# Performance work log

Measured on AMD Instinct MI355X. Metric: run time of the kernel, lower is better.

Reference implementation:

```python
import jax, jax.numpy as jnp
import numpy as np

DILATION = 6
KS = 3
N = KS * KS  # 9 kernel sample points
PAD = 1      # zero padding inside DeformConv2d
EPS = 1e-5


def conv2d(x, w, b=None, padding=0):
    out = jax.lax.conv_general_dilated(
        x, w, window_strides=(1, 1),
        padding=[(padding, padding), (padding, padding)],
        dimension_numbers=('NCHW', 'OIHW', 'NCHW'))
    if b is not None:
        out = out + b[None, :, None, None]
    return out


def batchnorm_train(x, gamma, beta):
    # training-mode BN (module default): batch statistics over (N,H,W)
    mean = x.mean(axis=(0, 2, 3), keepdims=True)
    var = x.var(axis=(0, 2, 3), keepdims=True)
    return gamma[None, :, None, None] * (x - mean) * jax.lax.rsqrt(var + EPS) + beta[None, :, None, None]


def deform_conv(x, p_w, p_b, m_w, m_b, d_w, d_b, w):
    b, c, h, wd = x.shape
    offset = conv2d(x, p_w, p_b, padding=1)                 # (b, 2N, h, w)
    m = jax.nn.sigmoid(conv2d(x, m_w, m_b, padding=1))      # (b, N, h, w) modulation
    s = 2.0 * jax.nn.sigmoid(conv2d(x, d_w, d_b, padding=1))  # (b,1,h,w) adaptive dilation scale (=1 at logit 0)
    xp = jnp.pad(x, ((0, 0), (0, 0), (PAD, PAD), (PAD, PAD)))
    Hp, Wp = h + 2 * PAD, wd + 2 * PAD
    # kernel grid p_n, row-major (kh, kw) to match conv weight layout
    rng = jnp.arange(-(KS - 1) // 2, (KS - 1) // 2 + 1, dtype=x.dtype)
    pn_x, pn_y = jnp.meshgrid(rng, rng, indexing='ij')
    pn_x, pn_y = pn_x.reshape(-1), pn_y.reshape(-1)          # (N,)
    # base sampling positions (offset by PAD into padded map)
    p0_x = jnp.arange(1, h + 1, dtype=x.dtype)[:, None, None]    # (h,1,1)
    p0_y = jnp.arange(1, wd + 1, dtype=x.dtype)[None, :, None]   # (1,w,1)
    off = offset.transpose(0, 2, 3, 1)   # (b,h,w,2N)
    s_ = s.transpose(0, 2, 3, 1)         # (b,h,w,1)
    px = p0_x + DILATION * s_ * pn_x + off[..., :N]   # (b,h,w,N)
    py = p0_y + DILATION * s_ * pn_y + off[..., N:]
    fx, fy = jnp.floor(px), jnp.floor(py)
    qx_lt = jnp.clip(fx, 0, Hp - 1).astype(jnp.int32)
    qy_lt = jnp.clip(fy, 0, Wp - 1).astype(jnp.int32)
    qx_rb = jnp.clip(fx + 1, 0, Hp - 1).astype(jnp.int32)
    qy_rb = jnp.clip(fy + 1, 0, Wp - 1).astype(jnp.int32)
    pxc = jnp.clip(px, 0, Hp - 1)
    pyc = jnp.clip(py, 0, Wp - 1)
    g_lt = (1 + (qx_lt - pxc)) * (1 + (qy_lt - pyc))
    g_rb = (1 - (qx_rb - pxc)) * (1 - (qy_rb - pyc))
    g_lb = (1 + (qx_lt - pxc)) * (1 - (qy_rb - pyc))
    g_rt = (1 - (qx_rb - pxc)) * (1 + (qy_lt - pyc))

    def gather(qx, qy):
        idx = (qx * Wp + qy).reshape(b, 1, -1)                    # (b,1,h*w*N)
        xf = xp.reshape(b, c, Hp * Wp)
        out = jnp.take_along_axis(xf, jnp.broadcast_to(idx, (b, c, idx.shape[-1])), axis=2)
        return out.reshape(b, c, h, wd, N)

    x_off = (g_lt[:, None] * gather(qx_lt, qy_lt)
             + g_rb[:, None] * gather(qx_rb, qy_rb)
             + g_lb[:, None] * gather(qx_lt, qy_rb)
             + g_rt[:, None] * gather(qx_rb, qy_lt))
    x_off = x_off * m.transpose(0, 2, 3, 1)[:, None]              # modulation
    # final 3x3 conv over gathered samples == contraction over (c, N)
    return jnp.einsum('bchwn,ocn->bohw', x_off, w.reshape(w.shape[0], c, N))


def setup_inputs() -> dict:
    key = jax.random.key(0)
    ks = jax.random.split(key, 12)
    cin, c1, c2 = 512, 256, 64
    b, h, w = 2, 96, 96
    def rn(k, shape, scale):
        return jax.random.normal(k, shape, dtype=jnp.float32) * scale
    return {
        'x': rn(ks[0], (b, cin, h, w), 1.0),
        'bn1_g': jnp.ones((cin,), jnp.float32),
        'bn1_b': jnp.zeros((cin,), jnp.float32),
        'conv1_w': rn(ks[1], (c1, cin, 1, 1), (1.0 / cin) ** 0.5),
        'conv1_b': jnp.zeros((c1,), jnp.float32),
        'bn2_g': jnp.ones((c1,), jnp.float32),
        'bn2_b': jnp.zeros((c1,), jnp.float32),
        'p_w': rn(ks[2], (2 * N, c1, 3, 3), 0.01),
        'p_b': jnp.zeros((2 * N,), jnp.float32),
        'm_w': rn(ks[3], (N, c1, 3, 3), 0.01),
        'm_b': jnp.zeros((N,), jnp.float32),
        'd_w': rn(ks[4], (1, c1, 3, 3), 0.01),
        'd_b': jnp.zeros((1,), jnp.float32),
        'dconv_w': rn(ks[5], (c2, c1, 3, 3), (1.0 / (c1 * 9)) ** 0.5),
    }


def reference(x, bn1_g, bn1_b, conv1_w, conv1_b, bn2_g, bn2_b,
              p_w, p_b, m_w, m_b, d_w, d_b, dconv_w):
    f = jax.nn.relu(batchnorm_train(x, bn1_g, bn1_b))
    f = conv2d(f, conv1_w, conv1_b)
    f = batchnorm_train(f, bn2_g, bn2_b)
    return deform_conv(f, p_w, p_b, m_w, m_b, d_w, d_b, dconv_w)
```

## Files before the change

### kernel.cpp

```cpp
#include <hip/hip_runtime.h>
#include <hip/hip_bf16.h>
#include <math.h>

#define BATCH 2
#define CIN 512
#define C1 256
#define C2 64
#define HH 96
#define WW 96
#define HWSZ 9216
#define NPIX 18432
#define HP 98
#define WP 98
#define PLSTRIDE 516096

typedef __attribute__((ext_vector_type(8))) short bf16x8;
typedef __attribute__((ext_vector_type(4))) short bf16x4;
typedef __attribute__((ext_vector_type(4))) float f32x4;
typedef __attribute__((ext_vector_type(4))) unsigned int u32x4;
typedef __attribute__((ext_vector_type(2))) unsigned int u32x2;
typedef unsigned short u16;
typedef unsigned int u32;

__device__ __forceinline__ float bfu2f(u16 u) {
  u32 v = ((u32)u) << 16; return __builtin_bit_cast(float, v);
}
__device__ __forceinline__ u16 f2bfu(float f) {
  return __builtin_bit_cast(u16, __float2bfloat16(f));
}
__device__ __forceinline__ float rd_any(const void* p, size_t i, int fl) {
  return fl ? bfu2f(((const u16*)p)[i]) : ((const float*)p)[i];
}
__device__ __forceinline__ int get_fl(const u32* g1raw) {
  return g1raw[0] != 0x3F800000u;
}
__device__ __forceinline__ bf16x8 lds_frag(const u16* p) {
  bf16x4 lo = *(const bf16x4*)p;
  bf16x4 hi = *(const bf16x4*)(p + 4);
  bf16x8 r;
  r[0] = lo[0]; r[1] = lo[1]; r[2] = lo[2]; r[3] = lo[3];
  r[4] = hi[0]; r[5] = hi[1]; r[6] = hi[2]; r[7] = hi[3];
  return r;
}
__device__ __forceinline__ void split4(const f32x4& v, u32x2& ph, u32x2& pl) {
  u16 h0 = f2bfu(v[0]), h1 = f2bfu(v[1]), h2 = f2bfu(v[2]), h3 = f2bfu(v[3]);
  u16 l0 = f2bfu(v[0] - bfu2f(h0)), l1 = f2bfu(v[1] - bfu2f(h1));
  u16 l2 = f2bfu(v[2] - bfu2f(h2)), l3 = f2bfu(v[3] - bfu2f(h3));
  ph = (u32x2){(u32)h0 | ((u32)h1 << 16), (u32)h2 | ((u32)h3 << 16)};
  pl = (u32x2){(u32)l0 | ((u32)l1 << 16), (u32)l2 | ((u32)l3 << 16)};
}

__global__ __launch_bounds__(256) void prep_kernel(
    const void* cw, const void* pw, const void* mw, const void* dw, const void* dcw,
    const void* cb, const void* g1, const void* b1, const void* g2, const void* b2,
    const void* pb, const void* mb, const void* db,
    u16* __restrict__ W1b, u16* __restrict__ W1l,
    u16* __restrict__ Wofa, u16* __restrict__ Wofal,
    u16* __restrict__ Wab, u16* __restrict__ Wabl,
    float* __restrict__ canon, float* __restrict__ statz) {
  int e = blockIdx.x * 256 + threadIdx.x;
  if (e >= 356380) return;
  int fl = get_fl((const u32*)g1);
  if (e < 131072) {
    float v = rd_any(cw, e, fl);
    u16 h = f2bfu(v);
    W1b[e] = h; W1l[e] = f2bfu(v - bfu2f(h));
  } else if (e < 204800) {
    int i = e - 131072;
    int tap = i >> 13; int r = i & 8191; int m = r >> 8; int c = r & 255;
    float v = 0.f;
    if (m < 18)       v = rd_any(pw, (size_t)(m * 256 + c) * 9 + tap, fl);
    else if (m < 27)  v = rd_any(mw, (size_t)((m - 18) * 256 + c) * 9 + tap, fl);
    else if (m == 27) v = rd_any(dw, (size_t)c * 9 + tap, fl);
    u16 h = f2bfu(v);
    Wofa[i] = h; Wofal[i] = f2bfu(v - bfu2f(h));
  } else if (e < 352256) {
    int i = e - 204800;
    int n = i >> 14; int r = i & 16383; int o = r >> 8; int c = r & 255;
    float v = rd_any(dcw, (size_t)(o * 256 + c) * 9 + n, fl);
    u16 h = f2bfu(v);
    Wab[i] = h; Wabl[i] = f2bfu(v - bfu2f(h));
  } else if (e < 354076) {
    int i = e - 352256;
    const void* src; int off;
    if      (i < 256)  { src = cb; off = i; }
    else if (i < 768)  { src = g1; off = i - 256; }
    else if (i < 1280) { src = b1; off = i - 768; }
    else if (i < 1536) { src = g2; off = i - 1280; }
    else if (i < 1792) { src = b2; off = i - 1536; }
    else if (i < 1810) { src = pb; off = i - 1792; }
    else if (i < 1819) { src = mb; off = i - 1810; }
    else               { src = db; off = i - 1819; }
    canon[i] = rd_any(src, off, fl);
  } else {
    statz[e - 354076] = 0.f;
  }
}

__global__ __launch_bounds__(256) void bn_stats_kernel(
    const void* __restrict__ x, const float* __restrict__ gamma,
    const float* __restrict__ beta, float* __restrict__ scale,
    float* __restrict__ shift, float* __restrict__ sums, float* __restrict__ sumsq,
    int* __restrict__ cnt, const u32* __restrict__ g1raw, int force, int C) {
  int c = blockIdx.x, part = blockIdx.y, tid = threadIdx.x;
  int fl = force ? 1 : get_fl(g1raw);
  int b = part >> 1, half = part & 1;
  size_t base = ((size_t)(b * C + c)) * HWSZ + half * (HWSZ / 2);
  float s = 0.f, q = 0.f;
  if (fl) {
    const u16* p = (const u16*)x + base;
    for (int i = tid; i < 576; i += 256) {
      u32x4 U = *(const u32x4*)(p + i * 8);
      #pragma unroll
      for (int k = 0; k < 4; ++k) {
        float v0 = bfu2f((u16)(U[k] & 0xffff));
        float v1 = bfu2f((u16)(U[k] >> 16));
        s += v0 + v1; q = fmaf(v0, v0, fmaf(v1, v1, q));
      }
    }
  } else {
    const float* p = (const float*)x + base;
    for (int i = tid; i < 1152; i += 256) {
      f32x4 v = *(const f32x4*)(p + i * 4);
      #pragma unroll
      for (int k = 0; k < 4; ++k) { s += v[k]; q = fmaf(v[k], v[k], q); }
    }
  }
  __shared__ float sh[512];
  sh[tid] = s; sh[tid + 256] = q;
  __syncthreads();
  for (int off = 128; off > 0; off >>= 1) {
    if (tid < off) { sh[tid] += sh[tid + off]; sh[tid + 256] += sh[tid + 256 + off]; }
    __syncthreads();
  }
  if (tid == 0) {
    atomicAdd(&sums[c], sh[0]);
    atomicAdd(&sumsq[c], sh[256]);
    __threadfence();
    int old = atomicAdd(&cnt[c], 1);
    if (old == 3) {
      float S = atomicAdd(&sums[c], 0.f);
      float Q = atomicAdd(&sumsq[c], 0.f);
      float mean = S * (1.f / (float)NPIX);
      float var  = fmaxf(Q * (1.f / (float)NPIX) - mean * mean, 0.f);
      float sc = gamma[c] * rsqrtf(var + 1e-5f);
      scale[c] = sc;
      shift[c] = beta[c] - mean * sc;
    }
  }
}

__global__ __launch_bounds__(256) void conv1x1_kernel(
    const void* __restrict__ x, const u16* __restrict__ W1b, const u16* __restrict__ W1l,
    const float* __restrict__ cb, const float* __restrict__ scale,
    const float* __restrict__ shift, const u32* __restrict__ g1raw,
    u16* __restrict__ f1) {
  __shared__ u16 Bh[2][64][68];
  __shared__ u16 Bl[2][64][68];
  int tid = threadIdx.x;
  int fl = get_fl(g1raw);
  int bxr = blockIdx.x;
  int bx = (bxr & 7) * 36 + (bxr >> 3);
  int p0 = bx * 64;
  int co0 = blockIdx.y * 128;
  int b = p0 / HWSZ;
  int hw0 = p0 % HWSZ;
  int lane = tid & 63, wv = tid >> 6, quad = lane >> 4, mr = lane & 15;
  int m0 = co0 + wv * 32;
  f32x4 acc[2][4];
  #pragma unroll
  for (int i = 0; i < 2; ++i)
    #pragma unroll
    for (int j = 0; j < 4; ++j) acc[i][j] = (f32x4){0.f, 0.f, 0.f, 0.f};

  int spx = tid & 63, cg = tid >> 6;
  int gpx = hw0 + spx;

  float pva[8], pvb[8];
  auto ISSUE = [&](int c0) {
    #pragma unroll
    for (int j = 0; j < 8; ++j) {
      int ci = c0 + cg * 16 + j * 2;
      if (fl) {
        const u16* xb = (const u16*)x;
        pva[j] = bfu2f(xb[((size_t)(b * CIN + ci)) * HWSZ + gpx]);
        pvb[j] = bfu2f(xb[((size_t)(b * CIN + ci + 1)) * HWSZ + gpx]);
      } else {
        const float* xf = (const float*)x;
        pva[j] = xf[((size_t)(b * CIN + ci)) * HWSZ + gpx];
        pvb[j] = xf[((size_t)(b * CIN + ci + 1)) * HWSZ + gpx];
      }
    }
  };
  auto COMBINE = [&](int buf, int c0) {
    #pragma unroll
    for (int j = 0; j < 8; ++j) {
      int ci = c0 + cg * 16 + j * 2;
      float v0 = fmaxf(fmaf(pva[j], scale[ci], shift[ci]), 0.f);
      float v1 = fmaxf(fmaf(pvb[j], scale[ci + 1], shift[ci + 1]), 0.f);
      u16 h0 = f2bfu(v0), h1 = f2bfu(v1);
      u16 l0 = f2bfu(v0 - bfu2f(h0)), l1 = f2bfu(v1 - bfu2f(h1));
      *(u32*)&Bh[buf][spx][cg * 16 + j * 2] = (u32)h0 | ((u32)h1 << 16);
      *(u32*)&Bl[buf][spx][cg * 16 + j * 2] = (u32)l0 | ((u32)l1 << 16);
    }
  };

  ISSUE(0);
  COMBINE(0, 0);
  for (int c8 = 0; c8 < 8; ++c8) {
    __syncthreads();
    if (c8 < 7) ISSUE((c8 + 1) * 64);
    int bsel = c8 & 1;
    int c0 = c8 * 64;
    #pragma unroll
    for (int kk2 = 0; kk2 < 2; ++kk2) {
      int kk = kk2 * 32;
      #pragma unroll
      for (int mf = 0; mf < 2; ++mf) {
        size_t wix = (size_t)(m0 + mf * 16 + mr) * CIN + c0 + kk + quad * 8;
        bf16x8 ah = *(const bf16x8*)(W1b + wix);
        bf16x8 al = *(const bf16x8*)(W1l + wix);
        #pragma unroll
        for (int nt = 0; nt < 4; ++nt) {
          bf16x8 bl = lds_frag(&Bl[bsel][nt * 16 + mr][kk + quad * 8]);
          bf16x8 bh = lds_frag(&Bh[bsel][nt * 16 + mr][kk + quad * 8]);
          acc[mf][nt] = __builtin_amdgcn_mfma_f32_16x16x32_bf16(ah, bl, acc[mf][nt], 0, 0, 0);
          acc[mf][nt] = __builtin_amdgcn_mfma_f32_16x16x32_bf16(al, bh, acc[mf][nt], 0, 0, 0);
          acc[mf][nt] = __builtin_amdgcn_mfma_f32_16x16x32_bf16(ah, bh, acc[mf][nt], 0, 0, 0);
        }
      }
    }
    if (c8 < 7) COMBINE(bsel ^ 1, (c8 + 1) * 64);
  }
  #pragma unroll
  for (int mf = 0; mf < 2; ++mf) {
    #pragma unroll
    for (int nt = 0; nt < 4; ++nt) {
      #pragma unroll
      for (int r = 0; r < 4; ++r) {
        int co = m0 + mf * 16 + quad * 4 + r;
        f1[((size_t)(b * C1 + co)) * HWSZ + hw0 + nt * 16 + mr] = f2bfu(acc[mf][nt][r] + cb[co]);
      }
    }
  }
}

__global__ __launch_bounds__(256) void bn2pad_kernel(
    const u16* __restrict__ f1, const float* __restrict__ scale,
    const float* __restrict__ shift, float* __restrict__ xpf) {
  int bid = blockIdx.x;
  int ht = bid % 144; int ct = (bid / 144) & 3; int b = bid / 576;
  int hw0 = ht * 64, c0 = ct * 64;
  __shared__ float t[64][65];
  int tid = threadIdx.x;
  #pragma unroll
  for (int it = 0; it < 16; ++it) {
    int e = it * 256 + tid;
    int p = e & 63, ci = e >> 6;
    float v = bfu2f(f1[((size_t)(b * C1 + c0 + ci)) * HWSZ + hw0 + p]);
    t[ci][p] = fmaf(v, scale[c0 + ci], shift[c0 + ci]);
  }
  __syncthreads();
  #pragma unroll
  for (int it = 0; it < 16; ++it) {
    int e = it * 256 + tid;
    int ci = e & 63, p = e >> 6;
    int hw = hw0 + p; int h = hw / WW; int w = hw % WW;
    xpf[(((size_t)(b * HP) + h + 1) * WP + w + 1) * C1 + c0 + ci] = t[ci][p];
  }
}

__global__ __launch_bounds__(256) void init_kernel(float* __restrict__ xpf) {
  int k = blockIdx.x * 256 + threadIdx.x;
  int ch = k & 255; int pxi = k >> 8;
  int bb = pxi / 388; int r = pxi % 388;
  int h, w;
  if (r < 98)      { h = 0;  w = r; }
  else if (r < 196){ h = 97; w = r - 98; }
  else if (r < 292){ h = r - 196 + 1; w = 0; }
  else             { h = r - 292 + 1; w = 97; }
  xpf[(((size_t)(bb * HP) + h) * WP + w) * C1 + ch] = 0.f;
}

__global__ __launch_bounds__(256) void offconv_kernel(
    const float* __restrict__ xpf, const u16* __restrict__ Wofa, const u16* __restrict__ Wofal,
    const float* __restrict__ pbc, const float* __restrict__ mbc,
    const float* __restrict__ dbc, float* __restrict__ opart3) {
  __shared__ u16 Vh[2][32][68];
  __shared__ u16 Vl[2][32][68];
  int tid = threadIdx.x;
  int bxr = blockIdx.x;
  int bx = (bxr & 7) * 72 + (bxr >> 3);
  int tg = blockIdx.y;
  int p0 = bx * 32;
  int b = p0 / HWSZ;
  int hw = p0 % HWSZ; int h0 = hw / WW; int w0 = hw % WW;
  int lane = tid & 63, wv = tid >> 6, quad = lane >> 4, mr = lane & 15;
  int m0 = (wv & 1) * 16;
  int ntile = wv >> 1;
  int srow = tid >> 4;
  int scol = (tid & 15) * 4;
  f32x4 acc = (f32x4){0.f, 0.f, 0.f, 0.f};

  f32x4 pv[2];
  auto ISSUE = [&](int it) {
    int tap = tg * 3 + (it >> 2);
    int th = tap / 3, tw = tap % 3;
    int c0 = (it & 3) * 64;
    const float* base = xpf + ((size_t)(b * HP + h0 + th) * WP + (w0 + tw)) * C1;
    #pragma unroll
    for (int pass = 0; pass < 2; ++pass) {
      int px = pass * 16 + srow;
      pv[pass] = *(const f32x4*)(base + (size_t)px * C1 + c0 + scol);
    }
  };
  auto COMBINE = [&](int buf) {
    #pragma unroll
    for (int pass = 0; pass < 2; ++pass) {
      int px = pass * 16 + srow;
      u32x2 ph, pl;
      split4(pv[pass], ph, pl);
      *(u32x2*)&Vh[buf][px][scol] = ph;
      *(u32x2*)&Vl[buf][px][scol] = pl;
    }
  };

  ISSUE(0);
  COMBINE(0);
  for (int it = 0; it < 12; ++it) {
    __syncthreads();
    if (it < 11) ISSUE(it + 1);
    int bsel = it & 1;
    int tap = tg * 3 + (it >> 2);
    int c0 = (it & 3) * 64;
    #pragma unroll
    for (int kk2 = 0; kk2 < 2; ++kk2) {
      int kof = kk2 * 32 + quad * 8;
      size_t wix = (size_t)(tap * 32 + m0 + mr) * C1 + c0 + kof;
      bf16x8 ah = *(const bf16x8*)(Wofa + wix);
      bf16x8 al = *(const bf16x8*)(Wofal + wix);
      bf16x8 bl = lds_frag(&Vl[bsel][ntile * 16 + mr][kof]);
      bf16x8 bh = lds_frag(&Vh[bsel][ntile * 16 + mr][kof]);
      acc = __builtin_amdgcn_mfma_f32_16x16x32_bf16(ah, bl, acc, 0, 0, 0);
      acc = __builtin_amdgcn_mfma_f32_16x16x32_bf16(al, bh, acc, 0, 0, 0);
      acc = __builtin_amdgcn_mfma_f32_16x16x32_bf16(ah, bh, acc, 0, 0, 0);
    }
    if (it < 11) COMBINE(bsel ^ 1);
  }
  float* plane = opart3 + (size_t)tg * PLSTRIDE;
  int px = ntile * 16 + mr;
  #pragma unroll
  for (int r = 0; r < 4; ++r) {
    int m = m0 + quad * 4 + r;
    if (m < 28) {
      float v = acc[r];
      if (tg == 0) v += (m < 18) ? pbc[m] : ((m < 27) ? mbc[m - 18] : dbc[0]);
      plane[(size_t)m * NPIX + p0 + px] = v;
    }
  }
}

__global__ __launch_bounds__(256) void deform_kernel(
    const float* __restrict__ xpf, const u16* __restrict__ Wab, const u16* __restrict__ Wabl,
    const float* __restrict__ opart3, float* __restrict__ planes3) {
  __shared__ u16   Vh[2][32][68];
  __shared__ u16   Vl[2][32][68];
  __shared__ int   smi[3][4][32];
  __shared__ float smw[3][4][32];
  int tid = threadIdx.x;
  int bxr = blockIdx.x;
  int bx = (bxr & 7) * 72 + (bxr >> 3);
  int g = blockIdx.y;
  int p0 = bx * 32;
  int b = p0 / HWSZ;
  int hw0 = p0 % HWSZ;

  if (tid < 96) {
    int nn = tid >> 5;
    int p = tid & 31;
    int n = g * 3 + nn;
    int bp = p0 + p;
    int hw = hw0 + p; int h = hw / WW; int w = hw % WW;
    const float* P0 = opart3;
    const float* P1 = opart3 + PLSTRIDE;
    const float* P2 = opart3 + 2 * PLSTRIDE;
    size_t iox = (size_t)n * NPIX + bp;
    size_t ioy = (size_t)(9 + n) * NPIX + bp;
    size_t iml = (size_t)(18 + n) * NPIX + bp;
    size_t isl = (size_t)27 * NPIX + bp;
    float offx = P0[iox] + P1[iox] + P2[iox];
    float offy = P0[ioy] + P1[ioy] + P2[ioy];
    float mlog = P0[iml] + P1[iml] + P2[iml];
    float slog = P0[isl] + P1[isl] + P2[isl];
    float mm = 1.f / (1.f + expf(-mlog));
    float s  = 2.f / (1.f + expf(-slog));
    float pnx = (float)(n / 3 - 1), pny = (float)(n % 3 - 1);
    float px = (float)(h + 1) + 6.f * s * pnx + offx;
    float py = (float)(w + 1) + 6.f * s * pny + offy;
    float fx = floorf(px), fy = floorf(py);
    float qxlt = fminf(fmaxf(fx, 0.f), 97.f);
    float qylt = fminf(fmaxf(fy, 0.f), 97.f);
    float qxrb = fminf(fmaxf(fx + 1.f, 0.f), 97.f);
    float qyrb = fminf(fmaxf(fy + 1.f, 0.f), 97.f);
    float pxc = fminf(fmaxf(px, 0.f), 97.f);
    float pyc = fminf(fmaxf(py, 0.f), 97.f);
    float glt = (1.f + (qxlt - pxc)) * (1.f + (qylt - pyc));
    float grb = (1.f - (qxrb - pxc)) * (1.f - (qyrb - pyc));
    float glb = (1.f + (qxlt - pxc)) * (1.f - (qyrb - pyc));
    float grt = (1.f - (qxrb - pxc)) * (1.f + (qylt - pyc));
    int ixlt = (int)qxlt, iylt = (int)qylt, ixrb = (int)qxrb, iyrb = (int)qyrb;
    int base = b * (HP * WP);
    smi[nn][0][p] = base + ixlt * WP + iylt;  smw[nn][0][p] = glt * mm;
    smi[nn][1][p] = base + ixrb * WP + iyrb;  smw[nn][1][p] = grb * mm;
    smi[nn][2][p] = base + ixlt * WP + iyrb;  smw[nn][2][p] = glb * mm;
    smi[nn][3][p] = base + ixrb * WP + iylt;  smw[nn][3][p] = grt * mm;
  }
  __syncthreads();

  int lane = tid & 63, wv = tid >> 6, quad = lane >> 4, mr = lane & 15;
  int m0 = wv * 16;
  int srow = tid >> 4;
  int scol = (tid & 15) * 4;
  f32x4 acc[2];
  acc[0] = (f32x4){0.f, 0.f, 0.f, 0.f};
  acc[1] = (f32x4){0.f, 0.f, 0.f, 0.f};

  f32x4 pv[2][4];
  auto ISSUE = [&](int it) {
    int nn = it >> 2; int c0 = (it & 3) * 64;
    #pragma unroll
    for (int pass = 0; pass < 2; ++pass) {
      int px = pass * 16 + srow;
      #pragma unroll
      for (int k = 0; k < 4; ++k)
        pv[pass][k] = *(const f32x4*)(xpf + (size_t)smi[nn][k][px] * C1 + c0 + scol);
    }
  };
  auto COMBINE = [&](int buf, int it) {
    int nn = it >> 2;
    #pragma unroll
    for (int pass = 0; pass < 2; ++pass) {
      int px = pass * 16 + srow;
      float w0 = smw[nn][0][px], w1 = smw[nn][1][px], w2 = smw[nn][2][px], w3 = smw[nn][3][px];
      f32x4 vc;
      #pragma unroll
      for (int j = 0; j < 4; ++j)
        vc[j] = fmaf(w0, pv[pass][0][j],
                fmaf(w1, pv[pass][1][j],
                fmaf(w2, pv[pass][2][j], w3 * pv[pass][3][j])));
      u32x2 ph, pl;
      split4(vc, ph, pl);
      *(u32x2*)&Vh[buf][px][scol] = ph;
      *(u32x2*)&Vl[buf][px][scol] = pl;
    }
  };

  ISSUE(0);
  COMBINE(0, 0);
  for (int it = 0; it < 12; ++it) {
    __syncthreads();
    if (it < 11) ISSUE(it + 1);
    int bsel = it & 1;
    int n = g * 3 + (it >> 2); int c0 = (it & 3) * 64;
    #pragma unroll
    for (int kk2 = 0; kk2 < 2; ++kk2) {
      int kof = kk2 * 32 + quad * 8;
      size_t wix = (size_t)(n * C2 + m0 + mr) * C1 + c0 + kof;
      bf16x8 ah = *(const bf16x8*)(Wab + wix);
      bf16x8 al = *(const bf16x8*)(Wabl + wix);
      #pragma unroll
      for (int nt = 0; nt < 2; ++nt) {
        bf16x8 bl = lds_frag(&Vl[bsel][nt * 16 + mr][kof]);
        bf16x8 bh = lds_frag(&Vh[bsel][nt * 16 + mr][kof]);
        acc[nt] = __builtin_amdgcn_mfma_f32_16x16x32_bf16(ah, bl, acc[nt], 0, 0, 0);
        acc[nt] = __builtin_amdgcn_mfma_f32_16x16x32_bf16(al, bh, acc[nt], 0, 0, 0);
        acc[nt] = __builtin_amdgcn_mfma_f32_16x16x32_bf16(ah, bh, acc[nt], 0, 0, 0);
      }
    }
    if (it < 11) COMBINE(bsel ^ 1, it + 1);
  }
  #pragma unroll
  for (int nt = 0; nt < 2; ++nt) {
    #pragma unroll
    for (int r = 0; r < 4; ++r) {
      int o = m0 + quad * 4 + r;
      planes3[((size_t)g * C2 + o) * NPIX + p0 + nt * 16 + mr] = acc[nt][r];
    }
  }
}

__global__ __launch_bounds__(256) void reduce_kernel(
    const float* __restrict__ planes3, const u32* __restrict__ g1raw,
    void* __restrict__ outv) {
  int t = blockIdx.x * 256 + threadIdx.x;
  int e4 = t * 4;
  int b = e4 / (C2 * HWSZ);
  int rem = e4 % (C2 * HWSZ);
  int o = rem / HWSZ;
  int hw = rem % HWSZ;
  size_t src = (size_t)o * NPIX + b * HWSZ + hw;
  f32x4 v0 = *(const f32x4*)(planes3 + src);
  f32x4 v1 = *(const f32x4*)(planes3 + (size_t)C2 * NPIX + src);
  f32x4 v2 = *(const f32x4*)(planes3 + 2 * (size_t)C2 * NPIX + src);
  f32x4 sum;
  #pragma unroll
  for (int j = 0; j < 4; ++j) sum[j] = v0[j] + v1[j] + v2[j];
  if (get_fl(g1raw)) {
    u16* ob = (u16*)outv;
    #pragma unroll
    for (int j = 0; j < 4; ++j) ob[e4 + j] = f2bfu(sum[j]);
  } else {
    *(f32x4*)((float*)outv + e4) = sum;
  }
}

extern "C" void kernel_launch(void* const* d_in, const int* in_sizes, int n_in,
                              void* d_out, int out_size, void* d_ws, size_t ws_size,
                              hipStream_t stream) {
  const void* x       = d_in[0];
  const void* bn1_g   = d_in[1];
  const void* bn1_b   = d_in[2];
  const void* conv1_w = d_in[3];
  const void* conv1_b = d_in[4];
  const void* bn2_g   = d_in[5];
  const void* bn2_b   = d_in[6];
  const void* p_w     = d_in[7];
  const void* p_b     = d_in[8];
  const void* m_w     = d_in[9];
  const void* m_b     = d_in[10];
  const void* d_w     = d_in[11];
  const void* d_b     = d_in[12];
  const void* dconv_w = d_in[13];
  const u32* g1raw = (const u32*)bn1_g;

  float* ws = (float*)d_ws;
  float* canon = ws + 16;
  float* cbc = canon + 0;
  float* g1c = canon + 256;
  float* b1c = canon + 768;
  float* g2c = canon + 1280;
  float* b2c = canon + 1536;
  float* pbc = canon + 1792;
  float* mbc = canon + 1810;
  float* dbc = canon + 1819;
  float* scale1 = ws + 1840;
  float* shift1 = ws + 2352;
  float* scale2 = ws + 2864;
  float* shift2 = ws + 3120;
  float* statz  = ws + 3376;
  float* sums1  = statz;
  float* sumsq1 = statz + 512;
  int*   cnt1   = (int*)(statz + 1024);
  float* sums2  = statz + 1536;
  float* sumsq2 = statz + 1792;
  int*   cnt2   = (int*)(statz + 2048);
  u16* W1b   = (u16*)(ws + 5680);
  u16* W1l   = (u16*)(ws + 71216);
  u16* Wofa  = (u16*)(ws + 136752);
  u16* Wofal = (u16*)(ws + 173616);
  u16* Wab   = (u16*)(ws + 210480);
  u16* Wabl  = (u16*)(ws + 284208);
  u16* f1    = (u16*)(ws + 357936);
  float* opart3 = ws + 357936;
  float* xpf    = ws + 2717232;
  float* planes3 = ws + 7634480;

  prep_kernel<<<1393, 256, 0, stream>>>(conv1_w, p_w, m_w, d_w, dconv_w,
                                        conv1_b, bn1_g, bn1_b, bn2_g, bn2_b,
                                        p_b, m_b, d_b,
                                        W1b, W1l, Wofa, Wofal, Wab, Wabl, canon, statz);
  bn_stats_kernel<<<dim3(CIN, 4), 256, 0, stream>>>(x, g1c, b1c, scale1, shift1,
                                                    sums1, sumsq1, cnt1, g1raw, 0, CIN);
  conv1x1_kernel<<<dim3(288, 2), 256, 0, stream>>>(x, W1b, W1l, cbc, scale1, shift1, g1raw, f1);
  bn_stats_kernel<<<dim3(C1, 4), 256, 0, stream>>>(f1, g2c, b2c, scale2, shift2,
                                                   sums2, sumsq2, cnt2, g1raw, 1, C1);
  bn2pad_kernel<<<1152, 256, 0, stream>>>(f1, scale2, shift2, xpf);
  init_kernel<<<776, 256, 0, stream>>>(xpf);
  offconv_kernel<<<dim3(576, 3), 256, 0, stream>>>(xpf, Wofa, Wofal, pbc, mbc, dbc, opart3);
  deform_kernel<<<dim3(576, 3), 256, 0, stream>>>(xpf, Wab, Wabl, opart3, planes3);
  reduce_kernel<<<1152, 256, 0, stream>>>(planes3, g1raw, d_out);
}
```

Before: 323.2 us.

## Prefetch two iterations ahead in offconv/deform and fold border init into prep

The offconv and deform kernels now keep two register sets of global loads in flight, issuing the load for iteration it+2 before the MFMA work of iteration it, to hide global-memory latency better. The init kernel that zeroes the padding border of xpf is merged into prep_kernel, which removes one launch. The deeper prefetch raises register pressure, particularly in deform_kernel where each set holds 8 f32x4 values per thread, and this could lower occupancy.

```diff
diff --git a/kernel.cpp b/kernel.cpp
--- a/kernel.cpp
+++ b/kernel.cpp
@@ -57,9 +57,9 @@
     u16* __restrict__ W1b, u16* __restrict__ W1l,
     u16* __restrict__ Wofa, u16* __restrict__ Wofal,
     u16* __restrict__ Wab, u16* __restrict__ Wabl,
-    float* __restrict__ canon, float* __restrict__ statz) {
+    float* __restrict__ canon, float* __restrict__ statz, float* __restrict__ xpf) {
   int e = blockIdx.x * 256 + threadIdx.x;
-  if (e >= 356380) return;
+  if (e >= 555036) return;
   int fl = get_fl((const u32*)g1);
   if (e < 131072) {
     float v = rd_any(cw, e, fl);
@@ -92,8 +92,18 @@
     else if (i < 1819) { src = mb; off = i - 1810; }
     else               { src = db; off = i - 1819; }
     canon[i] = rd_any(src, off, fl);
+  } else if (e < 356380) {
+    statz[e - 354076] = 0.f;
   } else {
-    statz[e - 354076] = 0.f;
+    int k = e - 356380;
+    int ch = k & 255; int pxi = k >> 8;
+    int bb = pxi / 388; int r = pxi % 388;
+    int h, w;
+    if (r < 98)      { h = 0;  w = r; }
+    else if (r < 196){ h = 97; w = r - 98; }
+    else if (r < 292){ h = r - 196 + 1; w = 0; }
+    else             { h = r - 292 + 1; w = 97; }
+    xpf[(((size_t)(bb * HP) + h) * WP + w) * C1 + ch] = 0.f;
   }
 }
 
@@ -268,18 +278,6 @@
     int hw = hw0 + p; int h = hw / WW; int w = hw % WW;
     xpf[(((size_t)(b * HP) + h + 1) * WP + w + 1) * C1 + c0 + ci] = t[ci][p];
   }
-}
-
-__global__ __launch_bounds__(256) void init_kernel(float* __restrict__ xpf) {
-  int k = blockIdx.x * 256 + threadIdx.x;
-  int ch = k & 255; int pxi = k >> 8;
-  int bb = pxi / 388; int r = pxi % 388;
-  int h, w;
-  if (r < 98)      { h = 0;  w = r; }
-  else if (r < 196){ h = 97; w = r - 98; }
-  else if (r < 292){ h = r - 196 + 1; w = 0; }
-  else             { h = r - 292 + 1; w = 97; }
-  xpf[(((size_t)(bb * HP) + h) * WP + w) * C1 + ch] = 0.f;
 }
 
 __global__ __launch_bounds__(256) void offconv_kernel(
@@ -302,8 +300,8 @@
   int scol = (tid & 15) * 4;
   f32x4 acc = (f32x4){0.f, 0.f, 0.f, 0.f};
 
-  f32x4 pv[2];
-  auto ISSUE = [&](int it) {
+  f32x4 pvA[2], pvB[2];
+  auto ISSUE = [&](f32x4 (&pv)[2], int it) {
     int tap = tg * 3 + (it >> 2);
     int th = tap / 3, tw = tap % 3;
     int c0 = (it & 3) * 64;
@@ -314,7 +312,7 @@
       pv[pass] = *(const f32x4*)(base + (size_t)px * C1 + c0 + scol);
     }
   };
-  auto COMBINE = [&](int buf) {
+  auto COMBINE = [&](f32x4 (&pv)[2], int buf) {
     #pragma unroll
     for (int pass = 0; pass < 2; ++pass) {
       int px = pass * 16 + srow;
@@ -324,13 +322,7 @@
       *(u32x2*)&Vl[buf][px][scol] = pl;
     }
   };
-
-  ISSUE(0);
-  COMBINE(0);
-  for (int it = 0; it < 12; ++it) {
-    __syncthreads();
-    if (it < 11) ISSUE(it + 1);
-    int bsel = it & 1;
+  auto MFMA_STEP = [&](int bsel, int it) {
     int tap = tg * 3 + (it >> 2);
     int c0 = (it & 3) * 64;
     #pragma unroll
@@ -345,7 +337,20 @@
       acc = __builtin_amdgcn_mfma_f32_16x16x32_bf16(al, bh, acc, 0, 0, 0);
       acc = __builtin_amdgcn_mfma_f32_16x16x32_bf16(ah, bh, acc, 0, 0, 0);
     }
-    if (it < 11) COMBINE(bsel ^ 1);
+  };
+
+  ISSUE(pvA, 0);
+  ISSUE(pvB, 1);
+  COMBINE(pvA, 0);
+  for (int it = 0; it < 12; it += 2) {
+    __syncthreads();
+    if (it + 2 < 12) ISSUE(pvA, it + 2);
+    MFMA_STEP(0, it);
+    COMBINE(pvB, 1);
+    __syncthreads();
+    if (it + 3 < 12) ISSUE(pvB, it + 3);
+    MFMA_STEP(1, it + 1);
+    if (it + 2 < 12) COMBINE(pvA, 0);
   }
   float* plane = opart3 + (size_t)tg * PLSTRIDE;
   int px = ntile * 16 + mr;
@@ -425,8 +430,8 @@
   acc[0] = (f32x4){0.f, 0.f, 0.f, 0.f};
   acc[1] = (f32x4){0.f, 0.f, 0.f, 0.f};
 
-  f32x4 pv[2][4];
-  auto ISSUE = [&](int it) {
+  f32x4 pvA[2][4], pvB[2][4];
+  auto ISSUE = [&](f32x4 (&pv)[2][4], int it) {
     int nn = it >> 2; int c0 = (it & 3) * 64;
     #pragma unroll
     for (int pass = 0; pass < 2; ++pass) {
@@ -436,7 +441,7 @@
         pv[pass][k] = *(const f32x4*)(xpf + (size_t)smi[nn][k][px] * C1 + c0 + scol);
     }
   };
-  auto COMBINE = [&](int buf, int it) {
+  auto COMBINE = [&](f32x4 (&pv)[2][4], int buf, int it) {
     int nn = it >> 2;
     #pragma unroll
     for (int pass = 0; pass < 2; ++pass) {
@@ -454,13 +459,7 @@
       *(u32x2*)&Vl[buf][px][scol] = pl;
     }
   };
-
-  ISSUE(0);
-  COMBINE(0, 0);
-  for (int it = 0; it < 12; ++it) {
-    __syncthreads();
-    if (it < 11) ISSUE(it + 1);
-    int bsel = it & 1;
+  auto MFMA_STEP = [&](int bsel, int it) {
     int n = g * 3 + (it >> 2); int c0 = (it & 3) * 64;
     #pragma unroll
     for (int kk2 = 0; kk2 < 2; ++kk2) {
@@ -477,7 +476,20 @@
         acc[nt] = __builtin_amdgcn_mfma_f32_16x16x32_bf16(ah, bh, acc[nt], 0, 0, 0);
       }
     }
-    if (it < 11) COMBINE(bsel ^ 1, it + 1);
+  };
+
+  ISSUE(pvA, 0);
+  ISSUE(pvB, 1);
+  COMBINE(pvA, 0, 0);
+  for (int it = 0; it < 12; it += 2) {
+    __syncthreads();
+    if (it + 2 < 12) ISSUE(pvA, it + 2);
+    MFMA_STEP(0, it);
+    COMBINE(pvB, 1, it + 1);
+    __syncthreads();
+    if (it + 3 < 12) ISSUE(pvB, it + 3);
+    MFMA_STEP(1, it + 1);
+    if (it + 2 < 12) COMBINE(pvA, 0, it + 2);
   }
   #pragma unroll
   for (int nt = 0; nt < 2; ++nt) {
@@ -565,17 +577,16 @@
   float* xpf    = ws + 2717232;
   float* planes3 = ws + 7634480;
 
-  prep_kernel<<<1393, 256, 0, stream>>>(conv1_w, p_w, m_w, d_w, dconv_w,
+  prep_kernel<<<2169, 256, 0, stream>>>(conv1_w, p_w, m_w, d_w, dconv_w,
                                         conv1_b, bn1_g, bn1_b, bn2_g, bn2_b,
                                         p_b, m_b, d_b,
-                                        W1b, W1l, Wofa, Wofal, Wab, Wabl, canon, statz);
+                                        W1b, W1l, Wofa, Wofal, Wab, Wabl, canon, statz, xpf);
   bn_stats_kernel<<<dim3(CIN, 4), 256, 0, stream>>>(x, g1c, b1c, scale1, shift1,
                                                     sums1, sumsq1, cnt1, g1raw, 0, CIN);
   conv1x1_kernel<<<dim3(288, 2), 256, 0, stream>>>(x, W1b, W1l, cbc, scale1, shift1, g1raw, f1);
   bn_stats_kernel<<<dim3(C1, 4), 256, 0, stream>>>(f1, g2c, b2c, scale2, shift2,
                                                    sums2, sumsq2, cnt2, g1raw, 1, C1);
   bn2pad_kernel<<<1152, 256, 0, stream>>>(f1, scale2, shift2, xpf);
-  init_kernel<<<776, 256, 0, stream>>>(xpf);
   offconv_kernel<<<dim3(576, 3), 256, 0, stream>>>(xpf, Wofa, Wofal, pbc, mbc, dbc, opart3);
   deform_kernel<<<dim3(576, 3), 256, 0, stream>>>(xpf, Wab, Wabl, opart3, planes3);
   reduce_kernel<<<1152, 256, 0, stream>>>(planes3, g1raw, d_out);
```

New measurement: 311.9 us. -3.5%, faster.
